# Performance work log

Hardware: AMD Instinct MI355X
Metric: run time of the kernel (lower is better)

The kernel has to match this reference:

```python
import jax, jax.numpy as jnp
import numpy as np

TOP_K = 13
NUM_CLASSES = 80
ALPHA = 1.0
BETA = 6.0
EPS = 1e-9
IOU_EPS = 1e-7


def _ciou(box1, box2, eps=IOU_EPS):
    # box1: gt [B,M,1,4], box2: pred [B,1,A,4], corner format x1y1x2y2
    b1x1, b1y1, b1x2, b1y2 = jnp.split(box1, 4, axis=-1)
    b2x1, b2y1, b2x2, b2y2 = jnp.split(box2, 4, axis=-1)
    w1, h1 = b1x2 - b1x1, b1y2 - b1y1 + eps
    w2, h2 = b2x2 - b2x1, b2y2 - b2y1 + eps
    inter = (jnp.clip(jnp.minimum(b1x2, b2x2) - jnp.maximum(b1x1, b2x1), 0, None)
             * jnp.clip(jnp.minimum(b1y2, b2y2) - jnp.maximum(b1y1, b2y1), 0, None))
    union = w1 * h1 + w2 * h2 - inter + eps
    iou = inter / union
    cw = jnp.maximum(b1x2, b2x2) - jnp.minimum(b1x1, b2x1)  # enclosing box
    ch = jnp.maximum(b1y2, b2y2) - jnp.minimum(b1y1, b2y1)
    c2 = cw ** 2 + ch ** 2 + eps
    rho2 = ((b2x1 + b2x2 - b1x1 - b1x2) ** 2 + (b2y1 + b2y2 - b1y1 - b1y2) ** 2) / 4.0
    v = (4.0 / np.pi ** 2) * (jnp.arctan(w2 / h2) - jnp.arctan(w1 / h1)) ** 2
    alpha = v / (v - iou + (1.0 + eps))
    return (iou - (rho2 / c2 + v * alpha))[..., 0]  # [B,M,A]


def _assign(pred_cls, pred_bbox, anchor_points, gt_cls, gt_bbox, mask_gt):
    B, A, C = pred_cls.shape
    M = gt_bbox.shape[1]
    # --- anchors inside gt boxes: [B,M,A] ---
    lt, rb = gt_bbox[:, :, None, :2], gt_bbox[:, :, None, 2:]   # [B,M,1,2]
    xy = anchor_points[None, None]                               # [1,1,A,2]
    deltas = jnp.concatenate([xy - lt, rb - xy], axis=-1)        # [B,M,A,4]
    mask_in_gts = (deltas.min(-1) > EPS).astype(pred_bbox.dtype)
    mask = mask_in_gts * mask_gt                                 # mask_gt [B,M,1] broadcasts
    # --- box metrics: gather class scores at gt labels, full CIoU grid masked ---
    labels = gt_cls[..., 0].astype(jnp.int32)                    # [B,M]
    idx = jnp.broadcast_to(labels[:, None, :], (B, A, M))
    bbox_scores = jnp.take_along_axis(pred_cls, idx, axis=2).transpose(0, 2, 1) * mask
    overlaps = jnp.clip(_ciou(gt_bbox[:, :, None], pred_bbox[:, None]), 0, None) * mask
    align_metric = bbox_scores ** ALPHA * overlaps ** BETA       # [B,M,A]
    # --- top-k candidate selection (indices of masked-out gts forced to 0, dup counts zeroed) ---
    _, topk_idx = jax.lax.top_k(align_metric, TOP_K)             # [B,M,K]
    topk_mask = jnp.broadcast_to(mask_gt > 0, (B, M, TOP_K))
    topk_idx = jnp.where(topk_mask, topk_idx, 0)
    bi = jnp.arange(B)[:, None, None]
    mi = jnp.arange(M)[None, :, None]
    count = jnp.zeros((B, M, A), jnp.int32).at[bi, mi, topk_idx].add(1)
    mask_topk = jnp.where(count > 1, 0, count).astype(align_metric.dtype)
    mask_pos = mask_topk * mask_in_gts * mask_gt                 # [B,M,A]
    # --- resolve anchors claimed by multiple gts via max overlap ---
    fg = mask_pos.sum(-2)                                        # [B,A]
    is_max = jax.nn.one_hot(overlaps.argmax(1), M, dtype=mask_pos.dtype).transpose(0, 2, 1)
    mask_pos = jnp.where(fg[:, None, :] > 1, is_max, mask_pos)
    fg_mask = mask_pos.sum(-2)                                   # [B,A]
    target_gt_idx = mask_pos.argmax(-2)                          # [B,A]
    # --- gather targets ---
    flat = target_gt_idx + jnp.arange(B)[:, None] * M
    target_labels = labels.reshape(-1)[flat]                     # [B,A]
    target_bbox = gt_bbox.reshape(-1, 4)[flat]                   # [B,A,4]
    target_cls = jnp.where(fg_mask[..., None] > 0,
                           jax.nn.one_hot(target_labels, C, dtype=pred_cls.dtype), 0.0)
    # --- normalize scores by aligned metric ---
    align_metric = align_metric * mask_pos
    pos_align = align_metric.max(-1, keepdims=True)              # [B,M,1]
    pos_overlap = (overlaps * mask_pos).max(-1, keepdims=True)   # [B,M,1]
    norm = (align_metric * pos_overlap / (pos_align + EPS)).max(-2)[..., None]  # [B,A,1]
    target_cls = target_cls * norm
    return target_cls, target_bbox, fg_mask


def setup_inputs() -> dict:
    key = jax.random.key(0)
    ks = jax.random.split(key, 8)
    B, A, C, M = 16, 8400, 80, 32
    anchor_points = jax.random.uniform(ks[0], (A, 2)) * 80.0
    pred_cls = jax.random.uniform(ks[1], (B, A, C))  # sigmoid-like scores in [0,1)
    ctr = anchor_points[None] + jax.random.normal(ks[2], (B, A, 2)) * 2.0
    sz = jax.random.uniform(ks[3], (B, A, 2)) * 15.0 + 2.0
    pred_bbox = jnp.concatenate([ctr - sz / 2, ctr + sz / 2], axis=-1)
    gctr = jax.random.uniform(ks[4], (B, M, 2)) * 80.0
    gsz = jax.random.uniform(ks[5], (B, M, 2)) * 25.0 + 3.0
    gt_bbox = jnp.concatenate([gctr - gsz / 2, gctr + gsz / 2], axis=-1)
    gt_cls = jax.random.randint(ks[6], (B, M, 1), 0, C).astype(jnp.int64)
    mask_gt = (jax.random.uniform(ks[7], (B, M, 1)) < 0.8).astype(jnp.float32)
    return {"pred_cls": pred_cls, "pred_bbox": pred_bbox, "anchor_points": anchor_points,
            "gt_cls": gt_cls, "gt_bbox": gt_bbox, "mask_gt": mask_gt}


def reference(pred_cls, pred_bbox, anchor_points, gt_cls, gt_bbox, mask_gt):
    target_cls, target_bbox, fg_mask = _assign(pred_cls, pred_bbox, anchor_points,
                                               gt_cls, gt_bbox, mask_gt)
    return target_cls, target_bbox, fg_mask.astype(bool)
```

## Files before the change

### kernel.cpp

```cpp
#include <hip/hip_runtime.h>
#include <cstdint>
#include <cstddef>

#define BB 16
#define AA 8400
#define CC 80
#define MM 32
#define TOPK 13
#define NW 4
#define WORDS 264
#define CWORDS 66
#define CANCH (CWORDS * 32)

__device__ __forceinline__ float ciou_clip(
    float gx1, float gy1, float gx2, float gy2, float at1,
    float4 pb, float w2, float h2, float at2)
{
  const float w1 = gx2 - gx1, h1 = gy2 - gy1 + 1e-7f;
  const float iw = fmaxf(fminf(gx2, pb.z) - fmaxf(gx1, pb.x), 0.f);
  const float ih = fmaxf(fminf(gy2, pb.w) - fmaxf(gy1, pb.y), 0.f);
  const float inter = iw * ih;
  const float uni = w1*h1 + w2*h2 - inter + 1e-7f;
  const float iou = inter / uni;
  const float cw = fmaxf(gx2, pb.z) - fminf(gx1, pb.x);
  const float ch = fmaxf(gy2, pb.w) - fminf(gy1, pb.y);
  const float c2 = cw*cw + ch*ch + 1e-7f;
  const float rx = pb.x + pb.z - gx1 - gx2;
  const float ry = pb.y + pb.w - gy1 - gy2;
  const float rho2 = (rx*rx + ry*ry) * 0.25f;
  const float dv = at2 - at1;
  const float v = 0.4052847345693511f * dv * dv;
  const float alpha = v / (v - iou + (1.f + 1e-7f));
  return fmaxf(iou - (rho2 / c2 + v * alpha), 0.f);
}

__global__ __launch_bounds__(256) void k_mask(
    const float* __restrict__ anchors, const float* __restrict__ gt_bbox,
    const float* __restrict__ mask_gt, unsigned int* __restrict__ inmaskT,
    unsigned int* __restrict__ claim,
    unsigned int* __restrict__ pos_align, unsigned int* __restrict__ pos_ovl)
{
  const int b = blockIdx.y;
  __shared__ float4 s_mb[MM];
  if (threadIdx.x < MM) {
    const int m = threadIdx.x;
    const float4 g = reinterpret_cast<const float4*>(gt_bbox)[b*MM + m];
    s_mb[m] = (mask_gt[b*MM + m] > 0.f) ? g
              : make_float4(1e30f, 1e30f, -1e30f, -1e30f);
    if (blockIdx.x == 0) { pos_align[b*MM + m] = 0u; pos_ovl[b*MM + m] = 0u; }
  }
  __syncthreads();
  const int a = blockIdx.x*256 + threadIdx.x;
  const int wave = threadIdx.x >> 6, lane = threadIdx.x & 63;
  float2 xy = make_float2(-1e30f, -1e30f);
  if (a < AA) {
    xy = reinterpret_cast<const float2*>(anchors)[a];
    claim[b*AA + a] = 0u;
  }
  const int wslot = blockIdx.x*8 + wave*2;
  #pragma unroll
  for (int m = 0; m < MM; ++m) {
    const float4 g = s_mb[m];
    const float mind = fminf(fminf(xy.x - g.x, xy.y - g.y),
                             fminf(g.z - xy.x, g.w - xy.y));
    const unsigned long long bal = __ballot(mind > 1e-9f);
    unsigned int* wp = inmaskT + (size_t)(b*MM + m)*WORDS + wslot;
    if (lane == 0) wp[0] = (unsigned int)(bal & 0xffffffffull);
    if (lane == 1) wp[1] = (unsigned int)(bal >> 32);
  }
}

__global__ __launch_bounds__(256) void k_topk(
    const float* __restrict__ pred_cls, const float* __restrict__ pred_bbox,
    const float* __restrict__ anchors, const int* __restrict__ gt_cls,
    const float* __restrict__ gt_bbox, const float* __restrict__ mask_gt,
    const unsigned int* __restrict__ inmaskT, unsigned int* __restrict__ claim)
{
  const int m = blockIdx.x, b = blockIdx.y;
  if (mask_gt[b*MM + m] <= 0.f) return;
  const int wave = threadIdx.x >> 6, lane = threadIdx.x & 63;
  __shared__ unsigned short q[NW][CANCH];
  __shared__ uint2 s_top[NW][TOPK];

  const float4 gb = reinterpret_cast<const float4*>(gt_bbox)[b*MM + m];
  const float at1 = atanf((gb.z - gb.x) / (gb.w - gb.y + 1e-7f));
  const int lbl = gt_cls[b*MM + m];
  const float*  clsbase = pred_cls + (size_t)b*AA*CC;
  const float4* pbase   = reinterpret_cast<const float4*>(pred_bbox) + (size_t)b*AA;
  const float2* axy     = reinterpret_cast<const float2*>(anchors);

  float v[TOPK]; int id[TOPK];
  #pragma unroll
  for (int i = 0; i < TOPK; ++i) { v[i] = -1.f; id[i] = 0x7fffffff; }

  if (wave == 0) {
    const int a = lane;
    const float2 xy = axy[a];
    const float mind = fminf(fminf(xy.x - gb.x, xy.y - gb.y),
                             fminf(gb.z - xy.x, gb.w - xy.y));
    float val = 0.f;
    if (mind > 1e-9f) {
      const float4 pb = pbase[a];
      const float w2 = pb.z - pb.x, h2 = pb.w - pb.y + 1e-7f;
      const float at2 = atanf(w2 / h2);
      const float ov = ciou_clip(gb.x, gb.y, gb.z, gb.w, at1, pb, w2, h2, at2);
      const float o2 = ov * ov;
      val = clsbase[(size_t)a*CC + lbl] * (o2 * o2 * o2);
    }
    v[0] = val; id[0] = a;
  }

  const unsigned int* wrow = inmaskT + (size_t)(b*MM + m)*WORDS + wave*CWORDS;
  int qc = 0;
  #pragma unroll
  for (int it = 0; it < 2; ++it) {
    const int wi = it*64 + lane;
    unsigned int w = 0u;
    if (wi < CWORDS) w = wrow[wi];
    if (wave == 0 && wi < 2) w = 0u;
    const int cnt = __popc(w);
    int incl = cnt;
    #pragma unroll
    for (int off = 1; off < 64; off <<= 1) {
      const int t = __shfl_up(incl, off);
      if (lane >= off) incl += t;
    }
    int pos = qc + incl - cnt;
    const int abase = wave*CANCH + wi*32;
    unsigned int t = w;
    while (t) {
      const int bit = __ffs((int)t) - 1; t &= t - 1u;
      q[wave][pos++] = (unsigned short)(abase + bit);
    }
    qc += __shfl(incl, 63);
  }

  for (int k = lane; k < qc; k += 64) {
    const int a = (int)q[wave][k];
    const float4 pb = pbase[a];
    const float w2 = pb.z - pb.x, h2 = pb.w - pb.y + 1e-7f;
    const float at2 = atanf(w2 / h2);
    const float ov = ciou_clip(gb.x, gb.y, gb.z, gb.w, at1, pb, w2, h2, at2);
    const float o2 = ov * ov;
    const float val = clsbase[(size_t)a*CC + lbl] * (o2 * o2 * o2);
    if (val > v[TOPK-1] || (val == v[TOPK-1] && a < id[TOPK-1])) {
      #pragma unroll
      for (int i = TOPK-1; i >= 1; --i) {
        const bool ci = (val > v[i])   || (val == v[i]   && a < id[i]);
        const bool cp = (val > v[i-1]) || (val == v[i-1] && a < id[i-1]);
        if (ci) {
          if (cp) { v[i] = v[i-1]; id[i] = id[i-1]; }
          else    { v[i] = val;    id[i] = a; }
        }
      }
      if (val > v[0] || (val == v[0] && a < id[0])) { v[0] = val; id[0] = a; }
    }
  }

  for (int r = 0; r < TOPK; ++r) {
    float bv = v[0]; int bi = id[0];
    #pragma unroll
    for (int off = 32; off; off >>= 1) {
      const float ovv = __shfl_xor(bv, off);
      const int   oii = __shfl_xor(bi, off);
      if (ovv > bv || (ovv == bv && oii < bi)) { bv = ovv; bi = oii; }
    }
    if (v[0] == bv && id[0] == bi) {
      #pragma unroll
      for (int i = 0; i < TOPK-1; ++i) { v[i] = v[i+1]; id[i] = id[i+1]; }
      v[TOPK-1] = -1.f; id[TOPK-1] = 0x7fffffff;
    }
    if (lane == 0) s_top[wave][r] = make_uint2(__float_as_uint(bv), (unsigned)bi);
  }
  __syncthreads();
  if (wave != 0) return;

  float mv = -1.f; int mi = 0x7fffffff; bool ing = false;
  if (lane < NW*TOPK) {
    const uint2 c = s_top[lane/TOPK][lane%TOPK];
    mv = __uint_as_float(c.x); mi = (int)c.y;
    if (mi < AA) {
      const float2 xy = axy[mi];
      const float mind = fminf(fminf(xy.x - gb.x, xy.y - gb.y),
                               fminf(gb.z - xy.x, gb.w - xy.y));
      ing = mind > 1e-9f;
    }
  }
  const unsigned int bit = 1u << m;
  for (int r = 0; r < TOPK; ++r) {
    float bv = mv; int bi = mi;
    #pragma unroll
    for (int off = 32; off; off >>= 1) {
      const float ovv = __shfl_xor(bv, off);
      const int   oii = __shfl_xor(bi, off);
      if (ovv > bv || (ovv == bv && oii < bi)) { bv = ovv; bi = oii; }
    }
    const bool win = (mv == bv) && (mi == bi);
    if (win && ing) atomicOr(&claim[b*AA + bi], bit);
    if (win) { mv = -1.f; mi = 0x7fffffff; ing = false; }
  }
}

__global__ __launch_bounds__(256) void k_resolve(
    const float* __restrict__ pred_cls, const float* __restrict__ pred_bbox,
    const float* __restrict__ anchors, const int* __restrict__ gt_cls,
    const float* __restrict__ gt_bbox, const float* __restrict__ mask_gt,
    const unsigned int* __restrict__ claim,
    float* __restrict__ out_bbox, float* __restrict__ out_fg,
    int* __restrict__ anchor_m, float* __restrict__ anchor_al,
    unsigned int* __restrict__ pos_align, unsigned int* __restrict__ pos_ovl)
{
  const int b = blockIdx.y;
  __shared__ float s_x1[MM], s_y1[MM], s_x2[MM], s_y2[MM], s_at[MM], s_mgt[MM];
  __shared__ int s_lbl[MM];
  if (threadIdx.x < MM) {
    int m = threadIdx.x;
    float4 g = reinterpret_cast<const float4*>(gt_bbox)[b*MM + m];
    s_x1[m] = g.x; s_y1[m] = g.y; s_x2[m] = g.z; s_y2[m] = g.w;
    s_at[m] = atanf((g.z - g.x) / (g.w - g.y + 1e-7f));
    s_lbl[m] = gt_cls[b*MM + m];
    s_mgt[m] = mask_gt[b*MM + m];
  }
  __syncthreads();
  const int a = blockIdx.x*256 + threadIdx.x;
  if (a >= AA) return;
  const unsigned int cb = claim[b*AA + a];
  const int fg = __popc(cb);
  int asg = -1; float bestov = 0.f;
  if (fg > 0) {
    const float4 pb = reinterpret_cast<const float4*>(pred_bbox)[b*AA + a];
    const float2 xy = reinterpret_cast<const float2*>(anchors)[a];
    const float w2 = pb.z - pb.x, h2 = pb.w - pb.y + 1e-7f;
    const float at2 = atanf(w2 / h2);
    if (fg == 1) {
      asg = __ffs(cb) - 1;
      bestov = ciou_clip(s_x1[asg], s_y1[asg], s_x2[asg], s_y2[asg], s_at[asg],
                         pb, w2, h2, at2);
    } else {
      float best = -1.f; int bm = 0;
      for (int m = 0; m < MM; ++m) {
        float ov = 0.f;
        const float mind = fminf(fminf(xy.x - s_x1[m], xy.y - s_y1[m]),
                                 fminf(s_x2[m] - xy.x, s_y2[m] - xy.y));
        if (mind > 1e-9f && s_mgt[m] > 0.f)
          ov = ciou_clip(s_x1[m], s_y1[m], s_x2[m], s_y2[m], s_at[m],
                         pb, w2, h2, at2);
        if (ov > best) { best = ov; bm = m; }
      }
      asg = bm; bestov = best;
    }
  }
  const int tgt = (asg >= 0) ? asg : 0;
  float4 tb; tb.x = s_x1[tgt]; tb.y = s_y1[tgt]; tb.z = s_x2[tgt]; tb.w = s_y2[tgt];
  reinterpret_cast<float4*>(out_bbox)[b*AA + a] = tb;
  out_fg[b*AA + a] = (asg >= 0) ? 1.f : 0.f;
  anchor_m[b*AA + a] = asg;
  float av = 0.f;
  if (asg >= 0) {
    const float o2 = bestov * bestov;
    av = pred_cls[(size_t)(b*AA + a)*CC + s_lbl[asg]] * (o2 * o2 * o2);
    atomicMax(&pos_align[b*MM + asg], __float_as_uint(av));
    atomicMax(&pos_ovl[b*MM + asg], __float_as_uint(bestov));
  }
  anchor_al[b*AA + a] = av;
}

__global__ __launch_bounds__(256) void k_cls(
    const int* __restrict__ anchor_m, const float* __restrict__ anchor_al,
    const unsigned int* __restrict__ pos_align, const unsigned int* __restrict__ pos_ovl,
    const int* __restrict__ gt_cls, float* __restrict__ out_cls)
{
  const int tid = blockIdx.x*256 + threadIdx.x;
  if (tid >= BB*AA*(CC/4)) return;
  const int q  = tid % (CC/4);
  const int ba = tid / (CC/4);
  const int b  = ba / AA;
  const int m  = anchor_m[ba];
  float4 o = make_float4(0.f, 0.f, 0.f, 0.f);
  if (m >= 0) {
    const float pa = __uint_as_float(pos_align[b*MM + m]);
    const float po = __uint_as_float(pos_ovl[b*MM + m]);
    const float norm = anchor_al[ba] * po / (pa + 1e-9f);
    const int lbl = gt_cls[b*MM + m];
    const int c0 = q * 4;
    if (lbl == c0    ) o.x = norm;
    if (lbl == c0 + 1) o.y = norm;
    if (lbl == c0 + 2) o.z = norm;
    if (lbl == c0 + 3) o.w = norm;
  }
  reinterpret_cast<float4*>(out_cls)[tid] = o;
}

extern "C" void kernel_launch(void* const* d_in, const int* in_sizes, int n_in,
                              void* d_out, int out_size, void* d_ws, size_t ws_size,
                              hipStream_t stream)
{
  const float* pred_cls  = (const float*)d_in[0];
  const float* pred_bbox = (const float*)d_in[1];
  const float* anchors   = (const float*)d_in[2];
  const int*   gt_cls    = (const int*)  d_in[3];
  const float* gt_bbox   = (const float*)d_in[4];
  const float* mask_gt   = (const float*)d_in[5];

  char* ws = (char*)d_ws;
  unsigned int* claim     = (unsigned int*)(ws);
  unsigned int* pos_align = (unsigned int*)(ws + 537600);
  unsigned int* pos_ovl   = (unsigned int*)(ws + 539648);
  int*   anchor_m  = (int*)  (ws + 541696);
  float* anchor_al = (float*)(ws + 1079296);
  unsigned int* inmaskT = (unsigned int*)(ws + 1616896);

  float* out_cls  = (float*)d_out;
  float* out_bbox = out_cls + (size_t)BB*AA*CC;
  float* out_fg   = out_bbox + (size_t)BB*AA*4;

  k_mask<<<dim3(33, BB), 256, 0, stream>>>(
      anchors, gt_bbox, mask_gt, inmaskT, claim, pos_align, pos_ovl);
  k_topk<<<dim3(MM, BB), 256, 0, stream>>>(
      pred_cls, pred_bbox, anchors, gt_cls, gt_bbox, mask_gt, inmaskT, claim);
  k_resolve<<<dim3((AA + 255)/256, BB), 256, 0, stream>>>(
      pred_cls, pred_bbox, anchors, gt_cls, gt_bbox, mask_gt, claim,
      out_bbox, out_fg, anchor_m, anchor_al, pos_align, pos_ovl);
  k_cls<<<(BB*AA*(CC/4) + 255)/256, 256, 0, stream>>>(
      anchor_m, anchor_al, pos_align, pos_ovl, gt_cls, out_cls);
}
```

Before: 55.74 us.

## Double top-k waves per GT and pack score/index into 64-bit keys

The top-k kernel now uses 8 waves (512 threads) per GT box instead of 4. Each wave scans 33 mask words, so the two-pass prefix-scan loop collapses to a single pass. Score and anchor index are packed into one 64-bit key (score high, inverted index low), so each comparison and shuffle reduction handles a single integer instead of a float/int pair with tie-breaking. The final merge now covers 104 candidates at two per lane. The aim is more parallelism for the CIoU scoring, cheaper insertion and reduction, at the cost of more waves in the 13-round merge, larger register and LDS footprint, and reliance on scores being non-negative for key ordering.

```diff
diff --git a/kernel.cpp b/kernel.cpp
--- a/kernel.cpp
+++ b/kernel.cpp
@@ -7,9 +7,9 @@
 #define CC 80
 #define MM 32
 #define TOPK 13
-#define NW 4
+#define NW 8
 #define WORDS 264
-#define CWORDS 66
+#define CWORDS 33
 #define CANCH (CWORDS * 32)
 
 __device__ __forceinline__ float ciou_clip(
@@ -34,6 +34,14 @@
   return fmaxf(iou - (rho2 / c2 + v * alpha), 0.f);
 }
 
+__device__ __forceinline__ unsigned long long pack_key(float val, int a) {
+  return ((unsigned long long)__float_as_uint(val) << 32)
+       | (unsigned long long)(0xFFFFFFFFu - (unsigned)a);
+}
+__device__ __forceinline__ int key_anchor(unsigned long long k) {
+  return (int)(0xFFFFFFFFu - (unsigned)(k & 0xFFFFFFFFull));
+}
+
 __global__ __launch_bounds__(256) void k_mask(
     const float* __restrict__ anchors, const float* __restrict__ gt_bbox,
     const float* __restrict__ mask_gt, unsigned int* __restrict__ inmaskT,
@@ -70,7 +78,7 @@
   }
 }
 
-__global__ __launch_bounds__(256) void k_topk(
+__global__ __launch_bounds__(512) void k_topk(
     const float* __restrict__ pred_cls, const float* __restrict__ pred_bbox,
     const float* __restrict__ anchors, const int* __restrict__ gt_cls,
     const float* __restrict__ gt_bbox, const float* __restrict__ mask_gt,
@@ -80,7 +88,7 @@
   if (mask_gt[b*MM + m] <= 0.f) return;
   const int wave = threadIdx.x >> 6, lane = threadIdx.x & 63;
   __shared__ unsigned short q[NW][CANCH];
-  __shared__ uint2 s_top[NW][TOPK];
+  __shared__ unsigned long long s_top[NW][TOPK];
 
   const float4 gb = reinterpret_cast<const float4*>(gt_bbox)[b*MM + m];
   const float at1 = atanf((gb.z - gb.x) / (gb.w - gb.y + 1e-7f));
@@ -89,9 +97,9 @@
   const float4* pbase   = reinterpret_cast<const float4*>(pred_bbox) + (size_t)b*AA;
   const float2* axy     = reinterpret_cast<const float2*>(anchors);
 
-  float v[TOPK]; int id[TOPK];
+  unsigned long long k13[TOPK];
   #pragma unroll
-  for (int i = 0; i < TOPK; ++i) { v[i] = -1.f; id[i] = 0x7fffffff; }
+  for (int i = 0; i < TOPK; ++i) k13[i] = 0ull;
 
   if (wave == 0) {
     const int a = lane;
@@ -107,97 +115,99 @@
       const float o2 = ov * ov;
       val = clsbase[(size_t)a*CC + lbl] * (o2 * o2 * o2);
     }
-    v[0] = val; id[0] = a;
+    k13[0] = pack_key(val, a);
   }
 
   const unsigned int* wrow = inmaskT + (size_t)(b*MM + m)*WORDS + wave*CWORDS;
-  int qc = 0;
+  unsigned int w = 0u;
+  if (lane < CWORDS) w = wrow[lane];
+  if (wave == 0 && lane < 2) w = 0u;
+  const int cnt = __popc(w);
+  int incl = cnt;
   #pragma unroll
-  for (int it = 0; it < 2; ++it) {
-    const int wi = it*64 + lane;
-    unsigned int w = 0u;
-    if (wi < CWORDS) w = wrow[wi];
-    if (wave == 0 && wi < 2) w = 0u;
-    const int cnt = __popc(w);
-    int incl = cnt;
-    #pragma unroll
-    for (int off = 1; off < 64; off <<= 1) {
-      const int t = __shfl_up(incl, off);
-      if (lane >= off) incl += t;
-    }
-    int pos = qc + incl - cnt;
-    const int abase = wave*CANCH + wi*32;
+  for (int off = 1; off < 64; off <<= 1) {
+    const int t = __shfl_up(incl, off);
+    if (lane >= off) incl += t;
+  }
+  int pos = incl - cnt;
+  {
+    const int lbase = lane*32;
     unsigned int t = w;
     while (t) {
       const int bit = __ffs((int)t) - 1; t &= t - 1u;
-      q[wave][pos++] = (unsigned short)(abase + bit);
-    }
-    qc += __shfl(incl, 63);
-  }
-
+      q[wave][pos++] = (unsigned short)(lbase + bit);
+    }
+  }
+  const int qc = __shfl(incl, 63);
+
+  const int abase = wave * CANCH;
   for (int k = lane; k < qc; k += 64) {
-    const int a = (int)q[wave][k];
+    const int a = abase + (int)q[wave][k];
     const float4 pb = pbase[a];
     const float w2 = pb.z - pb.x, h2 = pb.w - pb.y + 1e-7f;
     const float at2 = atanf(w2 / h2);
     const float ov = ciou_clip(gb.x, gb.y, gb.z, gb.w, at1, pb, w2, h2, at2);
     const float o2 = ov * ov;
     const float val = clsbase[(size_t)a*CC + lbl] * (o2 * o2 * o2);
-    if (val > v[TOPK-1] || (val == v[TOPK-1] && a < id[TOPK-1])) {
+    const unsigned long long key = pack_key(val, a);
+    if (key > k13[TOPK-1]) {
       #pragma unroll
-      for (int i = TOPK-1; i >= 1; --i) {
-        const bool ci = (val > v[i])   || (val == v[i]   && a < id[i]);
-        const bool cp = (val > v[i-1]) || (val == v[i-1] && a < id[i-1]);
-        if (ci) {
-          if (cp) { v[i] = v[i-1]; id[i] = id[i-1]; }
-          else    { v[i] = val;    id[i] = a; }
-        }
-      }
-      if (val > v[0] || (val == v[0] && a < id[0])) { v[0] = val; id[0] = a; }
+      for (int i = TOPK-1; i >= 1; --i)
+        if (key > k13[i]) k13[i] = (key > k13[i-1]) ? k13[i-1] : key;
+      if (key > k13[0]) k13[0] = key;
     }
   }
 
   for (int r = 0; r < TOPK; ++r) {
-    float bv = v[0]; int bi = id[0];
+    unsigned long long bk = k13[0];
     #pragma unroll
     for (int off = 32; off; off >>= 1) {
-      const float ovv = __shfl_xor(bv, off);
-      const int   oii = __shfl_xor(bi, off);
-      if (ovv > bv || (ovv == bv && oii < bi)) { bv = ovv; bi = oii; }
-    }
-    if (v[0] == bv && id[0] == bi) {
+      const unsigned long long o = __shfl_xor(bk, off);
+      if (o > bk) bk = o;
+    }
+    if (k13[0] == bk) {
       #pragma unroll
-      for (int i = 0; i < TOPK-1; ++i) { v[i] = v[i+1]; id[i] = id[i+1]; }
-      v[TOPK-1] = -1.f; id[TOPK-1] = 0x7fffffff;
-    }
-    if (lane == 0) s_top[wave][r] = make_uint2(__float_as_uint(bv), (unsigned)bi);
+      for (int i = 0; i < TOPK-1; ++i) k13[i] = k13[i+1];
+      k13[TOPK-1] = 0ull;
+    }
+    if (lane == 0) s_top[wave][r] = bk;
   }
   __syncthreads();
   if (wave != 0) return;
 
-  float mv = -1.f; int mi = 0x7fffffff; bool ing = false;
-  if (lane < NW*TOPK) {
-    const uint2 c = s_top[lane/TOPK][lane%TOPK];
-    mv = __uint_as_float(c.x); mi = (int)c.y;
-    if (mi < AA) {
-      const float2 xy = axy[mi];
-      const float mind = fminf(fminf(xy.x - gb.x, xy.y - gb.y),
-                               fminf(gb.z - xy.x, gb.w - xy.y));
-      ing = mind > 1e-9f;
+  unsigned long long v0 = 0ull, v1 = 0ull;
+  bool g0 = false, g1 = false;
+  {
+    const int e0 = lane, e1 = lane + 64;
+    v0 = s_top[e0/TOPK][e0%TOPK];
+    if (e1 < NW*TOPK) v1 = s_top[e1/TOPK][e1%TOPK];
+    const int a0 = key_anchor(v0), a1 = key_anchor(v1);
+    if ((unsigned)a0 < (unsigned)AA) {
+      const float2 xy = axy[a0];
+      g0 = fminf(fminf(xy.x - gb.x, xy.y - gb.y),
+                 fminf(gb.z - xy.x, gb.w - xy.y)) > 1e-9f;
+    }
+    if ((unsigned)a1 < (unsigned)AA) {
+      const float2 xy = axy[a1];
+      g1 = fminf(fminf(xy.x - gb.x, xy.y - gb.y),
+                 fminf(gb.z - xy.x, gb.w - xy.y)) > 1e-9f;
     }
   }
   const unsigned int bit = 1u << m;
   for (int r = 0; r < TOPK; ++r) {
-    float bv = mv; int bi = mi;
+    const bool s1 = v1 > v0;
+    unsigned long long bk = s1 ? v1 : v0;
+    const unsigned long long my = bk;
     #pragma unroll
     for (int off = 32; off; off >>= 1) {
-      const float ovv = __shfl_xor(bv, off);
-      const int   oii = __shfl_xor(bi, off);
-      if (ovv > bv || (ovv == bv && oii < bi)) { bv = ovv; bi = oii; }
-    }
-    const bool win = (mv == bv) && (mi == bi);
-    if (win && ing) atomicOr(&claim[b*AA + bi], bit);
-    if (win) { mv = -1.f; mi = 0x7fffffff; ing = false; }
+      const unsigned long long o = __shfl_xor(bk, off);
+      if (o > bk) bk = o;
+    }
+    if (my == bk && bk != 0ull) {
+      const bool ing = s1 ? g1 : g0;
+      if (ing) atomicOr(&claim[b*AA + key_anchor(bk)], bit);
+      if (s1) { v1 = 0ull; g1 = false; } else { v0 = 0ull; g0 = false; }
+    }
   }
 }
 
@@ -316,7 +326,7 @@
 
   k_mask<<<dim3(33, BB), 256, 0, stream>>>(
       anchors, gt_bbox, mask_gt, inmaskT, claim, pos_align, pos_ovl);
-  k_topk<<<dim3(MM, BB), 256, 0, stream>>>(
+  k_topk<<<dim3(MM, BB), 512, 0, stream>>>(
       pred_cls, pred_bbox, anchors, gt_cls, gt_bbox, mask_gt, inmaskT, claim);
   k_resolve<<<dim3((AA + 255)/256, BB), 256, 0, stream>>>(
       pred_cls, pred_bbox, anchors, gt_cls, gt_bbox, mask_gt, claim,
```

Result: faster. 50.01 us (-10.3%).
